# Optimization experiments

Measured on AMD Instinct MI355X. Metric: run time of the kernel, lower is better.

## Reference

```python
import math
import jax, jax.numpy as jnp
import numpy as np

NUM_HEADS = 4
HEAD_DIM = 384


def reshape_fortran(x, shape):
    # column-major (Fortran) reshape, matching the torch reverse-permute trick
    x = jnp.transpose(x, tuple(reversed(range(x.ndim))))
    x = x.reshape(tuple(reversed(shape)))
    return jnp.transpose(x, tuple(reversed(range(len(shape)))))


def rel_pos_rotate(data):
    # data: [b, n_heads, L=2M-1, S] -> [b, n_heads, S, S]
    data = jnp.transpose(data, (0, 2, 3, 1))  # [b, d0=L, d1=S, d2=H]
    b, d0, d1, d2 = data.shape
    data = jnp.concatenate([data, jnp.zeros((b, d1, d1, d2), data.dtype)], axis=1)
    data = reshape_fortran(data, (b, (d0 + d1) * d1, 1, d2))
    data = data[:, :(d1 + d0 - 1) * d1]
    data = reshape_fortran(data, (b, d0 + d1 - 1, d1, d2))
    n = d0 // 2
    data = jnp.swapaxes(data[:, n:n + d1], 1, 2)  # [b, d1, d1, d2]
    return jnp.transpose(data, (0, 3, 1, 2))      # [b, H, S, S]


def setup_inputs() -> dict:
    key = jax.random.key(0)
    ks = jax.random.split(key, 5)
    B, S, D = 4, 920, 1536
    M = 920
    return {
        "hidden_states": jax.random.normal(ks[0], (B, S, D), jnp.float32),
        "q_w": jax.random.normal(ks[1], (D, NUM_HEADS * HEAD_DIM), jnp.float32) * 0.02,
        "k_w": jax.random.normal(ks[2], (D, NUM_HEADS * HEAD_DIM), jnp.float32) * 0.02,
        "v_w": jax.random.normal(ks[3], (D, NUM_HEADS * HEAD_DIM), jnp.float32) * 0.02,
        "dist_emb": jax.random.normal(ks[4], (2 * M - 1, HEAD_DIM), jnp.float32) * 0.02,
    }


def reference(hidden_states, q_w, k_w, v_w, dist_emb):
    B, S, D = hidden_states.shape

    def heads(x):  # [B,S,H*hd] -> [B,H,S,hd]
        return jnp.transpose(x.reshape(B, S, NUM_HEADS, HEAD_DIM), (0, 2, 1, 3))

    # query is pre-scaled by 1/sqrt(head_dim), matching the torch code
    q = heads((hidden_states @ q_w) / math.sqrt(HEAD_DIM))
    k = heads(hidden_states @ k_w)
    v = heads(hidden_states @ v_w)

    scores = jnp.einsum("bhqd,bhkd->bhqk", q, k)  # [B,H,S,S]
    # relative position scores: [B,H,L,S] then skew-rotated into [B,H,S,S]
    rel = jnp.einsum("ld,bhsd->bhls", dist_emb, q)
    scores = scores + rel_pos_rotate(rel)

    probs = jax.nn.softmax(scores, axis=-1)
    ctx = jnp.einsum("bhqk,bhkd->bhqd", probs, v)  # [B,H,S,hd]
    ctx = jnp.transpose(ctx, (0, 2, 1, 3)).reshape(B, S, NUM_HEADS * HEAD_DIM)
    return ctx
```

## Files before the change

kernel.cpp:

```cpp
#include <hip/hip_runtime.h>
#include <cstdint>
#include <cstddef>

#define SEQ   920
#define DM    1536
#define DH    384
#define NHD   4
#define NB    4
#define NBH   16
#define MTOK  3680
#define NREL  1839

typedef short          bf16x8 __attribute__((ext_vector_type(8)));
typedef float          f32x4  __attribute__((ext_vector_type(4)));
typedef unsigned short u16x4  __attribute__((ext_vector_type(4)));
typedef unsigned short u16x8  __attribute__((ext_vector_type(8)));

__device__ __forceinline__ unsigned short f2bf(float f){
  union{float f; unsigned u;} v; v.f = f;
  unsigned r = v.u + 0x7FFFu + ((v.u >> 16) & 1u);
  return (unsigned short)(r >> 16);
}
__device__ __forceinline__ float bf2f(unsigned short h){
  union{unsigned u; float f;} v; v.u = ((unsigned)h) << 16;
  return v.f;
}
__device__ __forceinline__ f32x4 mfma_bf16(bf16x8 a, bf16x8 b, f32x4 c){
  return __builtin_amdgcn_mfma_f32_16x16x32_bf16(a, b, c, 0, 0, 0);
}
__device__ __forceinline__ void gload_lds16(const void* g, void* l){
  __builtin_amdgcn_global_load_lds((const __attribute__((address_space(1))) void*)g,
                                   (__attribute__((address_space(3))) void*)l, 16, 0, 0);
}

__global__ __launch_bounds__(256) void k_prep(const float* __restrict__ X,
                                              const float* __restrict__ de,
                                              const float* __restrict__ qw,
                                              const float* __restrict__ kw,
                                              const float* __restrict__ vw,
                                              unsigned short* __restrict__ Xb,
                                              unsigned short* __restrict__ Eb,
                                              unsigned short* __restrict__ Wt){
  __shared__ float t[32][33];
  int bid = blockIdx.x;
  if(bid < 6912){
    int z = bid / 2304, rem = bid % 2304;
    int k0 = (rem % 48) * 32, n0 = (rem / 48) * 32;
    const float* w = z == 0 ? qw : (z == 1 ? kw : vw);
    int tx = threadIdx.x & 31, ty = threadIdx.x >> 5;
    #pragma unroll
    for(int j = 0; j < 4; j++)
      t[ty*4+j][tx] = w[(size_t)(k0 + ty*4 + j) * DM + n0 + tx];
    __syncthreads();
    #pragma unroll
    for(int j = 0; j < 4; j++)
      Wt[(size_t)(z*DM + n0 + ty*4 + j) * DM + k0 + tx] = f2bf(t[tx][ty*4+j]);
  } else if(bid < 6912 + 2048){
    int i = ((bid - 6912) * 256 + threadIdx.x) * 4;
    const int n = MTOK*DM, stride = 2048 * 256 * 4;
    for(; i + 3 < n; i += stride){
      f32x4 v = *(const f32x4*)(X + i);
      u16x4 o; o.x = f2bf(v.x); o.y = f2bf(v.y); o.z = f2bf(v.z); o.w = f2bf(v.w);
      *(u16x4*)(Xb + i) = o;
    }
  } else {
    int i = ((bid - 6912 - 2048) * 256 + threadIdx.x) * 4;
    if(i + 3 < NREL*DH){
      f32x4 v = *(const f32x4*)(de + i);
      u16x4 o; o.x = f2bf(v.x); o.y = f2bf(v.y); o.z = f2bf(v.z); o.w = f2bf(v.w);
      *(u16x4*)(Eb + i) = o;
    }
  }
}

template<class Epi>
__device__ __forceinline__ void gemm192(const unsigned short* __restrict__ A, int lda, int Amax,
                                        const unsigned short* __restrict__ B, int ldb, int Bmax,
                                        int K, int m0, int n0, Epi epi){
  __shared__ unsigned short As[3*192*64];
  __shared__ unsigned short Bs[3*192*64];
  const int tid = threadIdx.x;
  const int w = tid >> 6, l = tid & 63;
  const int lg = l >> 4, lo = l & 15;
  const int wm = w >> 2, wn = w & 3;

  const char* ga[3]; const char* gb[3];
  #pragma unroll
  for(int r = 0; r < 3; r++){
    int row = r*64 + (tid >> 3);
    int gslot = (tid & 7) ^ (row & 7);
    int ar = m0 + row; ar = ar < Amax ? ar : Amax - 1;
    ga[r] = (const char*)A + (size_t)ar*lda*2 + gslot*16;
    int br = n0 + row; br = br < Bmax ? br : Bmax - 1;
    gb[r] = (const char*)B + (size_t)br*ldb*2 + gslot*16;
  }
  const int ldst = tid * 16;

  auto stage_pair = [&](int kt, int slot, int r){
    size_t koff = (size_t)kt * 128;
    gload_lds16(ga[r] + koff, (char*)As + slot*24576 + r*8192 + ldst);
    gload_lds16(gb[r] + koff, (char*)Bs + slot*24576 + r*8192 + ldst);
  };

  f32x4 acc[6][3] = {};
  const int sw = (lo & 7) << 4;
  const int nk = (2*K + 127) >> 7;
  const int tb = 2*K - (nk - 1)*128;
  const bool keep0 = (lg*16) < tb;
  const bool keep1 = (64 + lg*16) < tb;

  #pragma unroll
  for(int r = 0; r < 3; r++) stage_pair(0, 0, r);
  #pragma unroll
  for(int r = 0; r < 3; r++) stage_pair(1, 1, r);
  asm volatile("s_waitcnt vmcnt(6)" ::: "memory");
  __builtin_amdgcn_s_barrier();

  int st = 0;
  for(int t = 0; t < nk; t++){
    const bool last = (t == nk - 1);
    const bool pf = (t + 2 < nk);
    const int s2 = st + 2 >= 3 ? st - 1 : st + 2;
    const char* Ab = (const char*)As + st*24576;
    const char* Bb = (const char*)Bs + st*24576;

    bf16x8 bfr[3][2], afr[2][2];

    #pragma unroll
    for(int fj = 0; fj < 3; fj++){
      int row = wn*48 + fj*16 + lo;
      #pragma unroll
      for(int kk = 0; kk < 2; kk++)
        bfr[fj][kk] = *(const bf16x8*)(Bb + row*128 + ((kk*64 + lg*16) ^ sw));
    }
    #pragma unroll
    for(int fi = 0; fi < 2; fi++){
      int row = wm*96 + fi*16 + lo;
      #pragma unroll
      for(int kk = 0; kk < 2; kk++)
        afr[fi][kk] = *(const bf16x8*)(Ab + row*128 + ((kk*64 + lg*16) ^ sw));
    }
    if(pf) stage_pair(t + 2, s2, 0);
    if(last){
      #pragma unroll
      for(int fi = 0; fi < 2; fi++){
        if(!keep0) afr[fi][0] = bf16x8{};
        if(!keep1) afr[fi][1] = bf16x8{};
      }
    }
    __builtin_amdgcn_s_barrier();
    asm volatile("s_waitcnt lgkmcnt(0)" ::: "memory");
    __builtin_amdgcn_s_setprio(1);
    #pragma unroll
    for(int kk = 0; kk < 2; kk++)
      #pragma unroll
      for(int fi = 0; fi < 2; fi++)
        #pragma unroll
        for(int fj = 0; fj < 3; fj++)
          acc[fi][fj] = mfma_bf16(afr[fi][kk], bfr[fj][kk], acc[fi][fj]);
    __builtin_amdgcn_s_setprio(0);
    __builtin_amdgcn_s_barrier();

    #pragma unroll
    for(int fi = 0; fi < 2; fi++){
      int row = wm*96 + (fi + 2)*16 + lo;
      #pragma unroll
      for(int kk = 0; kk < 2; kk++)
        afr[fi][kk] = *(const bf16x8*)(Ab + row*128 + ((kk*64 + lg*16) ^ sw));
    }
    if(pf) stage_pair(t + 2, s2, 1);
    if(last){
      #pragma unroll
      for(int fi = 0; fi < 2; fi++){
        if(!keep0) afr[fi][0] = bf16x8{};
        if(!keep1) afr[fi][1] = bf16x8{};
      }
    }
    __builtin_amdgcn_s_barrier();
    asm volatile("s_waitcnt lgkmcnt(0)" ::: "memory");
    __builtin_amdgcn_s_setprio(1);
    #pragma unroll
    for(int kk = 0; kk < 2; kk++)
      #pragma unroll
      for(int fi = 0; fi < 2; fi++)
        #pragma unroll
        for(int fj = 0; fj < 3; fj++)
          acc[fi + 2][fj] = mfma_bf16(afr[fi][kk], bfr[fj][kk], acc[fi + 2][fj]);
    __builtin_amdgcn_s_setprio(0);
    __builtin_amdgcn_s_barrier();

    #pragma unroll
    for(int fi = 0; fi < 2; fi++){
      int row = wm*96 + (fi + 4)*16 + lo;
      #pragma unroll
      for(int kk = 0; kk < 2; kk++)
        afr[fi][kk] = *(const bf16x8*)(Ab + row*128 + ((kk*64 + lg*16) ^ sw));
    }
    if(pf){
      stage_pair(t + 2, s2, 2);
      asm volatile("s_waitcnt vmcnt(6)" ::: "memory");
    } else if(t + 1 < nk){
      asm volatile("s_waitcnt vmcnt(0)" ::: "memory");
    }
    if(last){
      #pragma unroll
      for(int fi = 0; fi < 2; fi++){
        if(!keep0) afr[fi][0] = bf16x8{};
        if(!keep1) afr[fi][1] = bf16x8{};
      }
    }
    __builtin_amdgcn_s_barrier();
    asm volatile("s_waitcnt lgkmcnt(0)" ::: "memory");
    __builtin_amdgcn_s_setprio(1);
    #pragma unroll
    for(int kk = 0; kk < 2; kk++)
      #pragma unroll
      for(int fi = 0; fi < 2; fi++)
        #pragma unroll
        for(int fj = 0; fj < 3; fj++)
          acc[fi + 4][fj] = mfma_bf16(afr[fi][kk], bfr[fj][kk], acc[fi + 4][fj]);
    __builtin_amdgcn_s_setprio(0);
    __builtin_amdgcn_s_barrier();

    st = st + 1 >= 3 ? 0 : st + 1;
  }

  #pragma unroll
  for(int fi = 0; fi < 6; fi++)
    #pragma unroll
    for(int fj = 0; fj < 3; fj++){
      int m = m0 + wm*96 + fi*16 + lg*4;
      int n = n0 + wn*48 + fj*16 + lo;
      epi(m, n, acc[fi][fj]);
    }
}

template<class Epi>
__device__ __forceinline__ void gemm256(const unsigned short* __restrict__ A, int lda, int Amax,
                                        const unsigned short* __restrict__ B, int ldb, int Bmax,
                                        int K, int m0, int n0, Epi epi){
  __shared__ char lds[131072];
  char* ldsA = lds;
  char* ldsB = lds + 65536;
  const int tid = threadIdx.x;
  const int w = tid >> 6, l = tid & 63;
  const int lg = l >> 4, lo = l & 15;
  const int wm = w >> 2, wn = w & 3;

  const int gcol = ((tid & 7) ^ ((tid >> 3) & 7)) * 16;
  const char* gA[2][2]; const char* gB[2][2];
  #pragma unroll
  for(int u = 0; u < 2; u++)
    #pragma unroll
    for(int j = 0; j < 2; j++){
      int ar = m0 + u*128 + j*64 + (tid >> 3); ar = ar < Amax ? ar : Amax - 1;
      gA[u][j] = (const char*)A + (size_t)ar*lda*2 + gcol;
      int br = n0 + u*128 + j*64 + (tid >> 3); br = br < Bmax ? br : Bmax - 1;
      gB[u][j] = (const char*)B + (size_t)br*ldb*2 + gcol;
    }
  auto stageA = [&](int kt, int s, int u){
    size_t koff = (size_t)kt * 128;
    #pragma unroll
    for(int j = 0; j < 2; j++)
      gload_lds16(gA[u][j] + koff, ldsA + s*32768 + u*16384 + j*8192 + tid*16);
  };
  auto stageB = [&](int kt, int s, int u){
    size_t koff = (size_t)kt * 128;
    #pragma unroll
    for(int j = 0; j < 2; j++)
      gload_lds16(gB[u][j] + koff, ldsB + s*32768 + u*16384 + j*8192 + tid*16);
  };

  f32x4 acc[2][4][4] = {};
  const int sw = (lo & 7) << 4;
  const int nk = K >> 6;

  stageB(0, 0, 0); stageB(0, 0, 1); stageA(0, 0, 0); stageA(0, 0, 1);
  asm volatile("s_waitcnt vmcnt(2)" ::: "memory");
  __builtin_amdgcn_s_barrier();

  for(int t = 0; t < nk; t++){
    const int s = t & 1, sn = s ^ 1;
    const bool pf = (t + 1 < nk);
    const char* Ab = ldsA + s*32768;
    const char* Bb = ldsB + s*32768;
    bf16x8 b0[4], b1[4], ar[4];

    #pragma unroll
    for(int fj = 0; fj < 4; fj++)
      b0[fj] = *(const bf16x8*)(Bb + (wn*64 + fj*16 + lo)*128 + ((lg*16) ^ sw));
    #pragma unroll
    for(int fi = 0; fi < 4; fi++)
      ar[fi] = *(const bf16x8*)(Ab + (wm*64 + fi*16 + lo)*128 + ((lg*16) ^ sw));
    if(pf) stageB(t + 1, sn, 0);
    __builtin_amdgcn_s_barrier();
    asm volatile("s_waitcnt lgkmcnt(0)" ::: "memory");
    __builtin_amdgcn_s_setprio(1);
    #pragma unroll
    for(int fi = 0; fi < 4; fi++)
      #pragma unroll
      for(int fj = 0; fj < 4; fj++)
        acc[0][fi][fj] = mfma_bf16(ar[fi], b0[fj], acc[0][fi][fj]);
    __builtin_amdgcn_s_setprio(0);

    #pragma unroll
    for(int fj = 0; fj < 4; fj++)
      b1[fj] = *(const bf16x8*)(Bb + (wn*64 + fj*16 + lo)*128 + ((64 + lg*16) ^ sw));
    #pragma unroll
    for(int fi = 0; fi < 4; fi++)
      ar[fi] = *(const bf16x8*)(Ab + (wm*64 + fi*16 + lo)*128 + ((64 + lg*16) ^ sw));
    if(pf){ stageB(t + 1, sn, 1);
            asm volatile("s_waitcnt vmcnt(4)" ::: "memory"); }
    else  { asm volatile("s_waitcnt vmcnt(0)" ::: "memory"); }
    __builtin_amdgcn_s_barrier();
    asm volatile("s_waitcnt lgkmcnt(0)" ::: "memory");
    __builtin_amdgcn_s_setprio(1);
    #pragma unroll
    for(int fi = 0; fi < 4; fi++)
      #pragma unroll
      for(int fj = 0; fj < 4; fj++)
        acc[0][fi][fj] = mfma_bf16(ar[fi], b1[fj], acc[0][fi][fj]);
    __builtin_amdgcn_s_setprio(0);

    #pragma unroll
    for(int fi = 0; fi < 4; fi++)
      ar[fi] = *(const bf16x8*)(Ab + (128 + wm*64 + fi*16 + lo)*128 + ((lg*16) ^ sw));
    if(pf) stageA(t + 1, sn, 0);
    __builtin_amdgcn_s_barrier();
    asm volatile("s_waitcnt lgkmcnt(0)" ::: "memory");
    __builtin_amdgcn_s_setprio(1);
    #pragma unroll
    for(int fi = 0; fi < 4; fi++)
      #pragma unroll
      for(int fj = 0; fj < 4; fj++)
        acc[1][fi][fj] = mfma_bf16(ar[fi], b0[fj], acc[1][fi][fj]);
    __builtin_amdgcn_s_setprio(0);

    #pragma unroll
    for(int fi = 0; fi < 4; fi++)
      ar[fi] = *(const bf16x8*)(Ab + (128 + wm*64 + fi*16 + lo)*128 + ((64 + lg*16) ^ sw));
    if(pf){ stageA(t + 1, sn, 1);
            asm volatile("s_waitcnt vmcnt(2)" ::: "memory"); }
    __builtin_amdgcn_s_barrier();
    asm volatile("s_waitcnt lgkmcnt(0)" ::: "memory");
    __builtin_amdgcn_s_setprio(1);
    #pragma unroll
    for(int fi = 0; fi < 4; fi++)
      #pragma unroll
      for(int fj = 0; fj < 4; fj++)
        acc[1][fi][fj] = mfma_bf16(ar[fi], b1[fj], acc[1][fi][fj]);
    __builtin_amdgcn_s_setprio(0);
  }

  #pragma unroll
  for(int lh = 0; lh < 2; lh++)
    #pragma unroll
    for(int fi = 0; fi < 4; fi++)
      #pragma unroll
      for(int fj = 0; fj < 4; fj++){
        int m = m0 + lh*128 + wm*64 + fi*16 + lg*4;
        int n = n0 + wn*64 + fj*16 + lo;
        epi(m, n, acc[lh][fi][fj]);
      }
}

__global__ __launch_bounds__(512) void k_proj(const unsigned short* __restrict__ X,
                                              const unsigned short* __restrict__ Wt,
                                              unsigned short* __restrict__ Qb,
                                              unsigned short* __restrict__ Kb,
                                              unsigned short* __restrict__ Vt){
  int bid = blockIdx.x;
  int wg  = (bid & 7) * 60 + (bid >> 3);
  int m0 = (wg % 20) * 192, n0 = (wg / 20) * 192;
  gemm192(X, DM, MTOK, Wt, DM, 3*DM, DM, m0, n0,
    [=] __device__ (int m, int n, f32x4 v4){
      if(m >= MTOK) return;
      int which = n / DM, r = n % DM, h = r / DH, d = r % DH;
      int b = m / SEQ, s = m % SEQ;
      int bh = b * NHD + h;
      if(which == 2){
        u16x4 o;
        o.x = f2bf(v4.x); o.y = f2bf(v4.y); o.z = f2bf(v4.z); o.w = f2bf(v4.w);
        *(u16x4*)(Vt + ((size_t)bh*DH + d)*SEQ + s) = o;
      } else if(which == 0){
        #pragma unroll
        for(int i = 0; i < 4; i++)
          Qb[((size_t)bh*SEQ + s + i)*DH + d] = f2bf(v4[i] * 0.05103103630798287f);
      } else {
        #pragma unroll
        for(int i = 0; i < 4; i++)
          Kb[((size_t)bh*SEQ + s + i)*DH + d] = f2bf(v4[i]);
      }
    });
}

__global__ __launch_bounds__(512) void k_rel(const unsigned short* __restrict__ Qb,
                                             const unsigned short* __restrict__ E,
                                             unsigned short* __restrict__ relS){
  int m0 = blockIdx.x * 192, n0 = blockIdx.y * 192;
  int s0 = m0 % SEQ;
  int qlo = s0, qhi = s0 + 191;
  if(qhi >= SEQ){ qlo = 0; qhi = SEQ - 1; }
  if(n0 + 191 < 919 - qhi || n0 > 1838 - qlo) return;
  gemm192(Qb, DH, NBH*SEQ, E, DH, NREL, DH, m0, n0,
    [=] __device__ (int m, int n, f32x4 v4){
      #pragma unroll
      for(int i = 0; i < 4; i++){
        int mi = m + i;
        if(mi >= NBH*SEQ) continue;
        int q = mi % SEQ;
        int j = n - 919 + q;
        if(j < 0 || j >= SEQ) continue;
        relS[(size_t)mi*SEQ + j] = f2bf(v4[i]);
      }
    });
}

__global__ __launch_bounds__(512, 2) void k_sgemm(const unsigned short* __restrict__ Qb,
                                                  const unsigned short* __restrict__ Kb,
                                                  unsigned short* __restrict__ P,
                                                  float* __restrict__ rs2){
  __shared__ float rsLds[256];
  if(threadIdx.x < 256) rsLds[threadIdx.x] = 0.f;
  int bid = blockIdx.x;
  int wg = (bid & 7) * 32 + (bid >> 3);
  int bh = wg >> 4, r = wg & 15;
  int m0 = (r & 3) * 256, n0 = (r >> 2) * 256;
  const unsigned short* A = Qb + (size_t)bh*SEQ*DH;
  const unsigned short* B = Kb + (size_t)bh*SEQ*DH;
  unsigned short* Pbh = P + (size_t)bh*SEQ*SEQ;
  const int lo = threadIdx.x & 15;
  gemm256(A, DH, SEQ, B, DH, SEQ, DH, m0, n0,
    [=] __device__ (int m, int n, f32x4 v4){
      float s[4];
      #pragma unroll
      for(int i = 0; i < 4; i++){
        int mi = m + i;
        float p = 0.f;
        if(mi < SEQ && n < SEQ){
          size_t off = (size_t)mi*SEQ + n;
          p = __expf(v4[i] + bf2f(Pbh[off]));
          Pbh[off] = f2bf(p);
        }
        s[i] = p;
      }
      #pragma unroll
      for(int i = 0; i < 4; i++){
        float v = s[i];
        v += __shfl_xor(v, 1); v += __shfl_xor(v, 2);
        v += __shfl_xor(v, 4); v += __shfl_xor(v, 8);
        if(lo == 0) atomicAdd(&rsLds[m - m0 + i], v);
      }
    });
  __syncthreads();
  if(threadIdx.x < 256){
    int row = m0 + threadIdx.x;
    if(row < SEQ) rs2[(((size_t)(n0 >> 8))*NBH + bh)*SEQ + row] = rsLds[threadIdx.x];
  }
}

__global__ __launch_bounds__(512) void k_pv(const unsigned short* __restrict__ P,
                                            const unsigned short* __restrict__ Vt,
                                            const float* __restrict__ rs2,
                                            float* __restrict__ out){
  int bid = blockIdx.x;
  int idp = (bid & 7) * 20 + (bid >> 3);
  int bh = idp / 10, r = idp % 10;
  int m0 = (r % 5) * 192, n0 = (r / 5) * 192;
  const unsigned short* A = P  + (size_t)bh*SEQ*SEQ;
  const unsigned short* B = Vt + (size_t)bh*DH*SEQ;
  const int b = bh >> 2, h = bh & 3;
  gemm192(A, SEQ, SEQ, B, SEQ, DH, SEQ, m0, n0,
    [=] __device__ (int m, int n, f32x4 v4){
      #pragma unroll
      for(int i = 0; i < 4; i++){
        int mi = m + i;
        if(mi >= SEQ) continue;
        float den = rs2[(size_t)bh*SEQ + mi]
                  + rs2[((size_t)1*NBH + bh)*SEQ + mi]
                  + rs2[((size_t)2*NBH + bh)*SEQ + mi]
                  + rs2[((size_t)3*NBH + bh)*SEQ + mi];
        out[((size_t)(b*SEQ + mi))*DM + h*DH + n] = v4[i] / den;
      }
    });
}

extern "C" void kernel_launch(void* const* d_in, const int* in_sizes, int n_in,
                              void* d_out, int out_size, void* d_ws, size_t ws_size,
                              hipStream_t stream){
  const float* X  = (const float*)d_in[0];
  const float* qw = (const float*)d_in[1];
  const float* kw = (const float*)d_in[2];
  const float* vw = (const float*)d_in[3];
  const float* de = (const float*)d_in[4];
  float* out = (float*)d_out;
  char* ws = (char*)d_ws;

  unsigned short* Qb   = (unsigned short*)ws;
  unsigned short* Kb   = (unsigned short*)(ws + 11304960);
  unsigned short* Vt   = (unsigned short*)(ws + 22609920);
  unsigned short* relS = (unsigned short*)(ws + 33914880);
  unsigned short* Eb   = (unsigned short*)(ws + 60999680);
  unsigned short* Xb   = (unsigned short*)(ws + 33914880);
  unsigned short* Wt   = (unsigned short*)(ws + 45219840);
  float*          rs2  = (float*)(ws + 60999680);

  k_prep<<<dim3(9650), dim3(256), 0, stream>>>(X, de, qw, kw, vw, Xb, Eb, Wt);
  k_proj<<<dim3(480), dim3(512), 0, stream>>>(Xb, Wt, Qb, Kb, Vt);
  k_rel<<<dim3(77,10), dim3(512), 0, stream>>>(Qb, Eb, relS);
  k_sgemm<<<dim3(256), dim3(512), 0, stream>>>(Qb, Kb, relS, rs2);
  k_pv<<<dim3(160), dim3(512), 0, stream>>>(relS, Vt, rs2, out);
}
```

Baseline: 219.2 us.

## Use 384x192 double-buffered GEMM tile for QKV projection

Adds a gemm384 routine that computes a 384x192 output tile per 512-thread block. Each warp owns a 96x96 sub-tile, and the A and B k-slices are double-buffered in 144KB of LDS. Global-to-LDS prefetches for the next k-step are interleaved across three MFMA phases. The projection launch drops from 480 to 240 blocks, so the grid fits in one wave on the CUs and more data is reused per tile. In exchange it uses much more LDS and more accumulator registers per thread, and the wait-count scheduling is fragile.

```diff
diff --git a/kernel.cpp b/kernel.cpp
--- a/kernel.cpp
+++ b/kernel.cpp
@@ -74,6 +74,135 @@
 }
 
 template<class Epi>
+__device__ __forceinline__ void gemm384(const unsigned short* __restrict__ A, int lda, int Amax,
+                                        const unsigned short* __restrict__ B, int ldb, int Bmax,
+                                        int K, int m0, int n0, Epi epi){
+  __shared__ char lds[147456];
+  char* ldsA = lds;
+  char* ldsB = lds + 98304;
+  const int tid = threadIdx.x;
+  const int w = tid >> 6, l = tid & 63;
+  const int lg = l >> 4, lo = l & 15;
+  const int wm = w >> 1, wn = w & 1;
+
+  const int gcol = ((tid & 7) ^ ((tid >> 3) & 7)) * 16;
+  const char* gA[6]; const char* gB[3];
+  #pragma unroll
+  for(int u = 0; u < 6; u++){
+    int ar = m0 + u*64 + (tid >> 3); ar = ar < Amax ? ar : Amax - 1;
+    gA[u] = (const char*)A + (size_t)ar*lda*2 + gcol;
+  }
+  #pragma unroll
+  for(int v = 0; v < 3; v++){
+    int br = n0 + v*64 + (tid >> 3); br = br < Bmax ? br : Bmax - 1;
+    gB[v] = (const char*)B + (size_t)br*ldb*2 + gcol;
+  }
+  auto stA = [&](int kt, int s, int u){
+    gload_lds16(gA[u] + (size_t)kt*128, ldsA + s*49152 + u*8192 + tid*16);
+  };
+  auto stB = [&](int kt, int s, int v){
+    gload_lds16(gB[v] + (size_t)kt*128, ldsB + s*24576 + v*8192 + tid*16);
+  };
+
+  f32x4 acc[6][6] = {};
+  const int sw = (lo & 7) << 4;
+  const int nk = K >> 6;
+
+  stA(0,0,0); stA(0,0,1); stA(0,0,3); stA(0,0,4);
+  stB(0,0,0); stB(0,0,1); stB(0,0,2);
+  stA(0,0,2); stA(0,0,5);
+  asm volatile("s_waitcnt vmcnt(2)" ::: "memory");
+  __builtin_amdgcn_s_barrier();
+
+  for(int t = 0; t < nk; t++){
+    const int s = t & 1, sn = s ^ 1;
+    const bool pf = (t + 1 < nk);
+    const char* Ab = ldsA + s*49152;
+    const char* Bb = ldsB + s*24576;
+    bf16x8 bfr[6][2], af[2][2];
+
+    #pragma unroll
+    for(int fj = 0; fj < 6; fj++){
+      int row = wn*96 + fj*16 + lo;
+      #pragma unroll
+      for(int kk = 0; kk < 2; kk++)
+        bfr[fj][kk] = *(const bf16x8*)(Bb + row*128 + ((kk*64 + lg*16) ^ sw));
+    }
+    #pragma unroll
+    for(int fi = 0; fi < 2; fi++){
+      int row = wm*96 + fi*16 + lo;
+      #pragma unroll
+      for(int kk = 0; kk < 2; kk++)
+        af[fi][kk] = *(const bf16x8*)(Ab + row*128 + ((kk*64 + lg*16) ^ sw));
+    }
+    if(pf){ stA(t+1,sn,0); stA(t+1,sn,1); stA(t+1,sn,3);
+            asm volatile("s_waitcnt vmcnt(3)" ::: "memory"); }
+    else  { asm volatile("s_waitcnt vmcnt(0)" ::: "memory"); }
+    __builtin_amdgcn_s_barrier();
+    asm volatile("s_waitcnt lgkmcnt(0)" ::: "memory");
+    __builtin_amdgcn_s_setprio(1);
+    #pragma unroll
+    for(int kk = 0; kk < 2; kk++)
+      #pragma unroll
+      for(int fi = 0; fi < 2; fi++)
+        #pragma unroll
+        for(int fj = 0; fj < 6; fj++)
+          acc[fi][fj] = mfma_bf16(af[fi][kk], bfr[fj][kk], acc[fi][fj]);
+    __builtin_amdgcn_s_setprio(0);
+
+    #pragma unroll
+    for(int fi = 0; fi < 2; fi++){
+      int row = wm*96 + (fi + 2)*16 + lo;
+      #pragma unroll
+      for(int kk = 0; kk < 2; kk++)
+        af[fi][kk] = *(const bf16x8*)(Ab + row*128 + ((kk*64 + lg*16) ^ sw));
+    }
+    if(pf){ stA(t+1,sn,4); stB(t+1,sn,0); stB(t+1,sn,1); }
+    __builtin_amdgcn_s_barrier();
+    asm volatile("s_waitcnt lgkmcnt(0)" ::: "memory");
+    __builtin_amdgcn_s_setprio(1);
+    #pragma unroll
+    for(int kk = 0; kk < 2; kk++)
+      #pragma unroll
+      for(int fi = 0; fi < 2; fi++)
+        #pragma unroll
+        for(int fj = 0; fj < 6; fj++)
+          acc[fi + 2][fj] = mfma_bf16(af[fi][kk], bfr[fj][kk], acc[fi + 2][fj]);
+    __builtin_amdgcn_s_setprio(0);
+
+    #pragma unroll
+    for(int fi = 0; fi < 2; fi++){
+      int row = wm*96 + (fi + 4)*16 + lo;
+      #pragma unroll
+      for(int kk = 0; kk < 2; kk++)
+        af[fi][kk] = *(const bf16x8*)(Ab + row*128 + ((kk*64 + lg*16) ^ sw));
+    }
+    if(pf){ stB(t+1,sn,2); stA(t+1,sn,2); stA(t+1,sn,5);
+            asm volatile("s_waitcnt vmcnt(2)" ::: "memory"); }
+    __builtin_amdgcn_s_barrier();
+    asm volatile("s_waitcnt lgkmcnt(0)" ::: "memory");
+    __builtin_amdgcn_s_setprio(1);
+    #pragma unroll
+    for(int kk = 0; kk < 2; kk++)
+      #pragma unroll
+      for(int fi = 0; fi < 2; fi++)
+        #pragma unroll
+        for(int fj = 0; fj < 6; fj++)
+          acc[fi + 4][fj] = mfma_bf16(af[fi][kk], bfr[fj][kk], acc[fi + 4][fj]);
+    __builtin_amdgcn_s_setprio(0);
+  }
+
+  #pragma unroll
+  for(int fi = 0; fi < 6; fi++)
+    #pragma unroll
+    for(int fj = 0; fj < 6; fj++){
+      int m = m0 + wm*96 + fi*16 + lg*4;
+      int n = n0 + wn*96 + fj*16 + lo;
+      epi(m, n, acc[fi][fj]);
+    }
+}
+
+template<class Epi>
 __device__ __forceinline__ void gemm192(const unsigned short* __restrict__ A, int lda, int Amax,
                                         const unsigned short* __restrict__ B, int ldb, int Bmax,
                                         int K, int m0, int n0, Epi epi){
@@ -364,15 +493,15 @@
       }
 }
 
-__global__ __launch_bounds__(512) void k_proj(const unsigned short* __restrict__ X,
-                                              const unsigned short* __restrict__ Wt,
-                                              unsigned short* __restrict__ Qb,
-                                              unsigned short* __restrict__ Kb,
-                                              unsigned short* __restrict__ Vt){
+__global__ __launch_bounds__(512, 2) void k_proj(const unsigned short* __restrict__ X,
+                                                 const unsigned short* __restrict__ Wt,
+                                                 unsigned short* __restrict__ Qb,
+                                                 unsigned short* __restrict__ Kb,
+                                                 unsigned short* __restrict__ Vt){
   int bid = blockIdx.x;
-  int wg  = (bid & 7) * 60 + (bid >> 3);
-  int m0 = (wg % 20) * 192, n0 = (wg / 20) * 192;
-  gemm192(X, DM, MTOK, Wt, DM, 3*DM, DM, m0, n0,
+  int wg  = (bid & 7) * 30 + (bid >> 3);
+  int m0 = (wg % 10) * 384, n0 = (wg / 10) * 192;
+  gemm384(X, DM, MTOK, Wt, DM, 3*DM, DM, m0, n0,
     [=] __device__ (int m, int n, f32x4 v4){
       if(m >= MTOK) return;
       int which = n / DM, r = n % DM, h = r / DH, d = r % DH;
@@ -506,7 +635,7 @@
   float*          rs2  = (float*)(ws + 60999680);
 
   k_prep<<<dim3(9650), dim3(256), 0, stream>>>(X, de, qw, kw, vw, Xb, Eb, Wt);
-  k_proj<<<dim3(480), dim3(512), 0, stream>>>(Xb, Wt, Qb, Kb, Vt);
+  k_proj<<<dim3(240), dim3(512), 0, stream>>>(Xb, Wt, Qb, Kb, Vt);
   k_rel<<<dim3(77,10), dim3(512), 0, stream>>>(Qb, Eb, relS);
   k_sgemm<<<dim3(256), dim3(512), 0, stream>>>(Qb, Kb, relS, rs2);
   k_pv<<<dim3(160), dim3(512), 0, stream>>>(relS, Vt, rs2, out);
```

Result: faster. 210.2 us (-4.1%).

## Use 384x192 GEMM tiles for projection and score kernels

Applied to the files above, without the earlier changes.

Adds a gemm384 routine with a 384x192 output tile and 8 waves laid out 4x2, each holding 6x6 accumulator fragments. The projection and QK^T score kernels now use it, which halves the projection grid to 240 blocks and sets the score grid to 240 blocks, while removing the old 256x256 gemm. The score kernel now writes five row-sum partials per row instead of four, and the PV kernel sums all five. The larger tiles are meant to cut redundant operand loads and give a grid of 240 blocks on the 256-CU part, but they use 144KB of LDS and more registers per wave. The prefetch now waits on the whole next stage at the end of each iteration, so load latency is overlapped less finely.

```diff
diff --git a/kernel.cpp b/kernel.cpp
--- a/kernel.cpp
+++ b/kernel.cpp
@@ -74,6 +74,129 @@
 }
 
 template<class Epi>
+__device__ __forceinline__ void gemm384(const unsigned short* __restrict__ A, int lda, int Amax,
+                                        const unsigned short* __restrict__ B, int ldb, int Bmax,
+                                        int K, int m0, int n0, Epi epi){
+  __shared__ char lds[147456];
+  char* ldsA = lds;
+  char* ldsB = lds + 98304;
+  const int tid = threadIdx.x;
+  const int w = tid >> 6, l = tid & 63;
+  const int lg = l >> 4, lo = l & 15;
+  const int wm = w >> 1, wn = w & 1;
+
+  const int gcol = ((tid & 7) ^ ((tid >> 3) & 7)) * 16;
+  const char* gA[6]; const char* gB[3];
+  #pragma unroll
+  for(int u = 0; u < 6; u++){
+    int ar = m0 + u*64 + (tid >> 3); ar = ar < Amax ? ar : Amax - 1;
+    gA[u] = (const char*)A + (size_t)ar*lda*2 + gcol;
+  }
+  #pragma unroll
+  for(int v = 0; v < 3; v++){
+    int br = n0 + v*64 + (tid >> 3); br = br < Bmax ? br : Bmax - 1;
+    gB[v] = (const char*)B + (size_t)br*ldb*2 + gcol;
+  }
+  auto stage_all = [&](int kt, int s){
+    size_t koff = (size_t)kt * 128;
+    #pragma unroll
+    for(int u = 0; u < 6; u++)
+      gload_lds16(gA[u] + koff, ldsA + s*49152 + u*8192 + tid*16);
+    #pragma unroll
+    for(int v = 0; v < 3; v++)
+      gload_lds16(gB[v] + koff, ldsB + s*24576 + v*8192 + tid*16);
+  };
+
+  f32x4 acc[6][6] = {};
+  const int sw = (lo & 7) << 4;
+  const int nk = K >> 6;
+
+  stage_all(0, 0);
+  asm volatile("s_waitcnt vmcnt(0)" ::: "memory");
+  __builtin_amdgcn_s_barrier();
+
+  for(int t = 0; t < nk; t++){
+    const int s = t & 1, sn = s ^ 1;
+    const bool pf = (t + 1 < nk);
+    const char* Ab = ldsA + s*49152;
+    const char* Bb = ldsB + s*24576;
+    bf16x8 b0[6], b1[6], af[3];
+
+    #pragma unroll
+    for(int fj = 0; fj < 6; fj++)
+      b0[fj] = *(const bf16x8*)(Bb + (wn*96 + fj*16 + lo)*128 + ((lg*16) ^ sw));
+    #pragma unroll
+    for(int fi = 0; fi < 3; fi++)
+      af[fi] = *(const bf16x8*)(Ab + (wm*96 + fi*16 + lo)*128 + ((lg*16) ^ sw));
+    if(pf) stage_all(t + 1, sn);
+    __builtin_amdgcn_s_barrier();
+    asm volatile("s_waitcnt lgkmcnt(0)" ::: "memory");
+    __builtin_amdgcn_s_setprio(1);
+    #pragma unroll
+    for(int fi = 0; fi < 3; fi++)
+      #pragma unroll
+      for(int fj = 0; fj < 6; fj++)
+        acc[fi][fj] = mfma_bf16(af[fi], b0[fj], acc[fi][fj]);
+    __builtin_amdgcn_s_setprio(0);
+
+    #pragma unroll
+    for(int fj = 0; fj < 6; fj++)
+      b1[fj] = *(const bf16x8*)(Bb + (wn*96 + fj*16 + lo)*128 + ((64 + lg*16) ^ sw));
+    #pragma unroll
+    for(int fi = 0; fi < 3; fi++)
+      af[fi] = *(const bf16x8*)(Ab + (wm*96 + fi*16 + lo)*128 + ((64 + lg*16) ^ sw));
+    __builtin_amdgcn_s_barrier();
+    asm volatile("s_waitcnt lgkmcnt(0)" ::: "memory");
+    __builtin_amdgcn_s_setprio(1);
+    #pragma unroll
+    for(int fi = 0; fi < 3; fi++)
+      #pragma unroll
+      for(int fj = 0; fj < 6; fj++)
+        acc[fi][fj] = mfma_bf16(af[fi], b1[fj], acc[fi][fj]);
+    __builtin_amdgcn_s_setprio(0);
+
+    #pragma unroll
+    for(int fi = 0; fi < 3; fi++)
+      af[fi] = *(const bf16x8*)(Ab + (wm*96 + (fi+3)*16 + lo)*128 + ((lg*16) ^ sw));
+    __builtin_amdgcn_s_barrier();
+    asm volatile("s_waitcnt lgkmcnt(0)" ::: "memory");
+    __builtin_amdgcn_s_setprio(1);
+    #pragma unroll
+    for(int fi = 0; fi < 3; fi++)
+      #pragma unroll
+      for(int fj = 0; fj < 6; fj++)
+        acc[fi+3][fj] = mfma_bf16(af[fi], b0[fj], acc[fi+3][fj]);
+    __builtin_amdgcn_s_setprio(0);
+
+    #pragma unroll
+    for(int fi = 0; fi < 3; fi++)
+      af[fi] = *(const bf16x8*)(Ab + (wm*96 + (fi+3)*16 + lo)*128 + ((64 + lg*16) ^ sw));
+    __builtin_amdgcn_s_barrier();
+    asm volatile("s_waitcnt lgkmcnt(0)" ::: "memory");
+    __builtin_amdgcn_s_setprio(1);
+    #pragma unroll
+    for(int fi = 0; fi < 3; fi++)
+      #pragma unroll
+      for(int fj = 0; fj < 6; fj++)
+        acc[fi+3][fj] = mfma_bf16(af[fi], b1[fj], acc[fi+3][fj]);
+    __builtin_amdgcn_s_setprio(0);
+    if(pf){
+      asm volatile("s_waitcnt vmcnt(0)" ::: "memory");
+      __builtin_amdgcn_s_barrier();
+    }
+  }
+
+  #pragma unroll
+  for(int fi = 0; fi < 6; fi++)
+    #pragma unroll
+    for(int fj = 0; fj < 6; fj++){
+      int m = m0 + wm*96 + fi*16 + lg*4;
+      int n = n0 + wn*96 + fj*16 + lo;
+      epi(m, n, acc[fi][fj]);
+    }
+}
+
+template<class Epi>
 __device__ __forceinline__ void gemm192(const unsigned short* __restrict__ A, int lda, int Amax,
                                         const unsigned short* __restrict__ B, int ldb, int Bmax,
                                         int K, int m0, int n0, Epi epi){
@@ -235,144 +358,15 @@
     }
 }
 
-template<class Epi>
-__device__ __forceinline__ void gemm256(const unsigned short* __restrict__ A, int lda, int Amax,
-                                        const unsigned short* __restrict__ B, int ldb, int Bmax,
-                                        int K, int m0, int n0, Epi epi){
-  __shared__ char lds[131072];
-  char* ldsA = lds;
-  char* ldsB = lds + 65536;
-  const int tid = threadIdx.x;
-  const int w = tid >> 6, l = tid & 63;
-  const int lg = l >> 4, lo = l & 15;
-  const int wm = w >> 2, wn = w & 3;
-
-  const int gcol = ((tid & 7) ^ ((tid >> 3) & 7)) * 16;
-  const char* gA[2][2]; const char* gB[2][2];
-  #pragma unroll
-  for(int u = 0; u < 2; u++)
-    #pragma unroll
-    for(int j = 0; j < 2; j++){
-      int ar = m0 + u*128 + j*64 + (tid >> 3); ar = ar < Amax ? ar : Amax - 1;
-      gA[u][j] = (const char*)A + (size_t)ar*lda*2 + gcol;
-      int br = n0 + u*128 + j*64 + (tid >> 3); br = br < Bmax ? br : Bmax - 1;
-      gB[u][j] = (const char*)B + (size_t)br*ldb*2 + gcol;
-    }
-  auto stageA = [&](int kt, int s, int u){
-    size_t koff = (size_t)kt * 128;
-    #pragma unroll
-    for(int j = 0; j < 2; j++)
-      gload_lds16(gA[u][j] + koff, ldsA + s*32768 + u*16384 + j*8192 + tid*16);
-  };
-  auto stageB = [&](int kt, int s, int u){
-    size_t koff = (size_t)kt * 128;
-    #pragma unroll
-    for(int j = 0; j < 2; j++)
-      gload_lds16(gB[u][j] + koff, ldsB + s*32768 + u*16384 + j*8192 + tid*16);
-  };
-
-  f32x4 acc[2][4][4] = {};
-  const int sw = (lo & 7) << 4;
-  const int nk = K >> 6;
-
-  stageB(0, 0, 0); stageB(0, 0, 1); stageA(0, 0, 0); stageA(0, 0, 1);
-  asm volatile("s_waitcnt vmcnt(2)" ::: "memory");
-  __builtin_amdgcn_s_barrier();
-
-  for(int t = 0; t < nk; t++){
-    const int s = t & 1, sn = s ^ 1;
-    const bool pf = (t + 1 < nk);
-    const char* Ab = ldsA + s*32768;
-    const char* Bb = ldsB + s*32768;
-    bf16x8 b0[4], b1[4], ar[4];
-
-    #pragma unroll
-    for(int fj = 0; fj < 4; fj++)
-      b0[fj] = *(const bf16x8*)(Bb + (wn*64 + fj*16 + lo)*128 + ((lg*16) ^ sw));
-    #pragma unroll
-    for(int fi = 0; fi < 4; fi++)
-      ar[fi] = *(const bf16x8*)(Ab + (wm*64 + fi*16 + lo)*128 + ((lg*16) ^ sw));
-    if(pf) stageB(t + 1, sn, 0);
-    __builtin_amdgcn_s_barrier();
-    asm volatile("s_waitcnt lgkmcnt(0)" ::: "memory");
-    __builtin_amdgcn_s_setprio(1);
-    #pragma unroll
-    for(int fi = 0; fi < 4; fi++)
-      #pragma unroll
-      for(int fj = 0; fj < 4; fj++)
-        acc[0][fi][fj] = mfma_bf16(ar[fi], b0[fj], acc[0][fi][fj]);
-    __builtin_amdgcn_s_setprio(0);
-
-    #pragma unroll
-    for(int fj = 0; fj < 4; fj++)
-      b1[fj] = *(const bf16x8*)(Bb + (wn*64 + fj*16 + lo)*128 + ((64 + lg*16) ^ sw));
-    #pragma unroll
-    for(int fi = 0; fi < 4; fi++)
-      ar[fi] = *(const bf16x8*)(Ab + (wm*64 + fi*16 + lo)*128 + ((64 + lg*16) ^ sw));
-    if(pf){ stageB(t + 1, sn, 1);
-            asm volatile("s_waitcnt vmcnt(4)" ::: "memory"); }
-    else  { asm volatile("s_waitcnt vmcnt(0)" ::: "memory"); }
-    __builtin_amdgcn_s_barrier();
-    asm volatile("s_waitcnt lgkmcnt(0)" ::: "memory");
-    __builtin_amdgcn_s_setprio(1);
-    #pragma unroll
-    for(int fi = 0; fi < 4; fi++)
-      #pragma unroll
-      for(int fj = 0; fj < 4; fj++)
-        acc[0][fi][fj] = mfma_bf16(ar[fi], b1[fj], acc[0][fi][fj]);
-    __builtin_amdgcn_s_setprio(0);
-
-    #pragma unroll
-    for(int fi = 0; fi < 4; fi++)
-      ar[fi] = *(const bf16x8*)(Ab + (128 + wm*64 + fi*16 + lo)*128 + ((lg*16) ^ sw));
-    if(pf) stageA(t + 1, sn, 0);
-    __builtin_amdgcn_s_barrier();
-    asm volatile("s_waitcnt lgkmcnt(0)" ::: "memory");
-    __builtin_amdgcn_s_setprio(1);
-    #pragma unroll
-    for(int fi = 0; fi < 4; fi++)
-      #pragma unroll
-      for(int fj = 0; fj < 4; fj++)
-        acc[1][fi][fj] = mfma_bf16(ar[fi], b0[fj], acc[1][fi][fj]);
-    __builtin_amdgcn_s_setprio(0);
-
-    #pragma unroll
-    for(int fi = 0; fi < 4; fi++)
-      ar[fi] = *(const bf16x8*)(Ab + (128 + wm*64 + fi*16 + lo)*128 + ((64 + lg*16) ^ sw));
-    if(pf){ stageA(t + 1, sn, 1);
-            asm volatile("s_waitcnt vmcnt(2)" ::: "memory"); }
-    __builtin_amdgcn_s_barrier();
-    asm volatile("s_waitcnt lgkmcnt(0)" ::: "memory");
-    __builtin_amdgcn_s_setprio(1);
-    #pragma unroll
-    for(int fi = 0; fi < 4; fi++)
-      #pragma unroll
-      for(int fj = 0; fj < 4; fj++)
-        acc[1][fi][fj] = mfma_bf16(ar[fi], b1[fj], acc[1][fi][fj]);
-    __builtin_amdgcn_s_setprio(0);
-  }
-
-  #pragma unroll
-  for(int lh = 0; lh < 2; lh++)
-    #pragma unroll
-    for(int fi = 0; fi < 4; fi++)
-      #pragma unroll
-      for(int fj = 0; fj < 4; fj++){
-        int m = m0 + lh*128 + wm*64 + fi*16 + lg*4;
-        int n = n0 + wn*64 + fj*16 + lo;
-        epi(m, n, acc[lh][fi][fj]);
-      }
-}
-
-__global__ __launch_bounds__(512) void k_proj(const unsigned short* __restrict__ X,
-                                              const unsigned short* __restrict__ Wt,
-                                              unsigned short* __restrict__ Qb,
-                                              unsigned short* __restrict__ Kb,
-                                              unsigned short* __restrict__ Vt){
+__global__ __launch_bounds__(512, 2) void k_proj(const unsigned short* __restrict__ X,
+                                                 const unsigned short* __restrict__ Wt,
+                                                 unsigned short* __restrict__ Qb,
+                                                 unsigned short* __restrict__ Kb,
+                                                 unsigned short* __restrict__ Vt){
   int bid = blockIdx.x;
-  int wg  = (bid & 7) * 60 + (bid >> 3);
-  int m0 = (wg % 20) * 192, n0 = (wg / 20) * 192;
-  gemm192(X, DM, MTOK, Wt, DM, 3*DM, DM, m0, n0,
+  int wg  = (bid & 7) * 30 + (bid >> 3);
+  int m0 = (wg % 10) * 384, n0 = (wg / 10) * 192;
+  gemm384(X, DM, MTOK, Wt, DM, 3*DM, DM, m0, n0,
     [=] __device__ (int m, int n, f32x4 v4){
       if(m >= MTOK) return;
       int which = n / DM, r = n % DM, h = r / DH, d = r % DH;
@@ -420,17 +414,17 @@
                                                   const unsigned short* __restrict__ Kb,
                                                   unsigned short* __restrict__ P,
                                                   float* __restrict__ rs2){
-  __shared__ float rsLds[256];
-  if(threadIdx.x < 256) rsLds[threadIdx.x] = 0.f;
+  __shared__ float rsLds[384];
+  if(threadIdx.x < 384) rsLds[threadIdx.x] = 0.f;
   int bid = blockIdx.x;
-  int wg = (bid & 7) * 32 + (bid >> 3);
-  int bh = wg >> 4, r = wg & 15;
-  int m0 = (r & 3) * 256, n0 = (r >> 2) * 256;
+  int wg = (bid & 7) * 30 + (bid >> 3);
+  int bh = wg / 15, r = wg % 15;
+  int m0 = (r % 3) * 384, n0 = (r / 3) * 192;
   const unsigned short* A = Qb + (size_t)bh*SEQ*DH;
   const unsigned short* B = Kb + (size_t)bh*SEQ*DH;
   unsigned short* Pbh = P + (size_t)bh*SEQ*SEQ;
   const int lo = threadIdx.x & 15;
-  gemm256(A, DH, SEQ, B, DH, SEQ, DH, m0, n0,
+  gemm384(A, DH, SEQ, B, DH, SEQ, DH, m0, n0,
     [=] __device__ (int m, int n, f32x4 v4){
       float s[4];
       #pragma unroll
@@ -453,9 +447,9 @@
       }
     });
   __syncthreads();
-  if(threadIdx.x < 256){
+  if(threadIdx.x < 384){
     int row = m0 + threadIdx.x;
-    if(row < SEQ) rs2[(((size_t)(n0 >> 8))*NBH + bh)*SEQ + row] = rsLds[threadIdx.x];
+    if(row < SEQ) rs2[(((size_t)(n0 / 192))*NBH + bh)*SEQ + row] = rsLds[threadIdx.x];
   }
 }
 
@@ -479,7 +473,8 @@
         float den = rs2[(size_t)bh*SEQ + mi]
                   + rs2[((size_t)1*NBH + bh)*SEQ + mi]
                   + rs2[((size_t)2*NBH + bh)*SEQ + mi]
-                  + rs2[((size_t)3*NBH + bh)*SEQ + mi];
+                  + rs2[((size_t)3*NBH + bh)*SEQ + mi]
+                  + rs2[((size_t)4*NBH + bh)*SEQ + mi];
         out[((size_t)(b*SEQ + mi))*DM + h*DH + n] = v4[i] / den;
       }
     });
@@ -506,8 +501,8 @@
   float*          rs2  = (float*)(ws + 60999680);
 
   k_prep<<<dim3(9650), dim3(256), 0, stream>>>(X, de, qw, kw, vw, Xb, Eb, Wt);
-  k_proj<<<dim3(480), dim3(512), 0, stream>>>(Xb, Wt, Qb, Kb, Vt);
+  k_proj<<<dim3(240), dim3(512), 0, stream>>>(Xb, Wt, Qb, Kb, Vt);
   k_rel<<<dim3(77,10), dim3(512), 0, stream>>>(Qb, Eb, relS);
-  k_sgemm<<<dim3(256), dim3(512), 0, stream>>>(Qb, Kb, relS, rs2);
+  k_sgemm<<<dim3(240), dim3(512), 0, stream>>>(Qb, Kb, relS, rs2);
   k_pv<<<dim3(160), dim3(512), 0, stream>>>(relS, Vt, rs2, out);
 }
```

After: 221.8 us. No clear change (+1.2%).
